# Performance work log

Hardware: AMD Instinct MI355X
Metric: run time of the kernel (lower is better)

## Reference

```python
import jax, jax.numpy as jnp
import numpy as np

B, E, H = 4096, 8, 1024
XDIM, ZDIM, ODIM, GH = 800, 64, 768, 128

def setup_inputs() -> dict:
    key = jax.random.key(0)
    ks = jax.random.split(key, 16)
    s = lambda k, shape, fan: jax.random.normal(k, shape, jnp.float32) / np.sqrt(fan)
    return {
        'x': jax.random.normal(ks[0], (B, XDIM), jnp.float32),
        'z': jax.random.normal(ks[1], (B, ZDIM), jnp.float32),
        'Wg1': s(ks[2], (GH, XDIM + ZDIM), XDIM + ZDIM),
        'bg1': jnp.zeros((GH,), jnp.float32),
        'Wg2': s(ks[3], (GH, GH), GH),
        'bg2': jnp.zeros((GH,), jnp.float32),
        'Wg3': s(ks[4], (E, GH), GH),
        'bg3': jnp.zeros((E,), jnp.float32),
        'W0': s(ks[5], (E, H, XDIM + ZDIM), XDIM + ZDIM),
        'b0': jnp.zeros((E, H), jnp.float32),
        'W1': s(ks[6], (E, H, H + ZDIM), H + ZDIM),
        'b1': jnp.zeros((E, H), jnp.float32),
        'W2': s(ks[7], (E, H, H + ZDIM), H + ZDIM),
        'b2': jnp.zeros((E, H), jnp.float32),
        'W3': s(ks[8], (E, ODIM, H), H),
        'b3': jnp.zeros((E, ODIM), jnp.float32),
    }

def _blended_layer(bc, inp, W, b):
    # equivalent to (sum_e bc_e W_e) @ inp + sum_e bc_e b_e, but computed as
    # per-expert matmul then weighted accumulation (avoids [B,out,in] blend).
    y = jnp.einsum('bi,eoi->beo', inp, W)          # per-expert outputs
    return jnp.einsum('be,beo->bo', bc, y) + bc @ b

def reference(x, z, Wg1, bg1, Wg2, bg2, Wg3, bg3,
              W0, b0, W1, b1, W2, b2, W3, b3):
    g = jnp.concatenate([x, z], axis=1)
    h = jax.nn.elu(g @ Wg1.T + bg1)
    h = jax.nn.elu(h @ Wg2.T + bg2)
    bc = jax.nn.softmax(h @ Wg3.T + bg3, axis=-1)  # [B, E] blend coefficients
    h = jax.nn.elu(_blended_layer(bc, jnp.concatenate([x, z], 1), W0, b0))
    h = jax.nn.elu(_blended_layer(bc, jnp.concatenate([h, z], 1), W1, b1))
    h = jax.nn.elu(_blended_layer(bc, jnp.concatenate([h, z], 1), W2, b2))
    return _blended_layer(bc, h, W3, b3)  # [B, ODIM], no activation
```

## Files before the change

kernel.cpp:

```cpp
#include <hip/hip_runtime.h>
#include <math.h>

#define BDIM 4096
#define NEXP 8
#define HDIM 1024
#define XDIM 800
#define ZDIM 64
#define ODIM 768
#define GH   128

typedef _Float16 f16;
typedef f16   f16x8 __attribute__((ext_vector_type(8)));
typedef f16   f16x4 __attribute__((ext_vector_type(4)));
typedef float f32x4 __attribute__((ext_vector_type(4)));

__device__ __forceinline__ float elu_act(float x) {
    return x > 0.0f ? x : expm1f(x);
}

__device__ __forceinline__ f16x8 vscale(f16x8 v, f16 s) {
    f16x8 r;
    #pragma unroll
    for (int i = 0; i < 8; ++i) r[i] = v[i] * s;
    return r;
}

#define BMg 64
#define BNg 64
#define BKg 32
#define PADg 68

template<int ACT>
__global__ __launch_bounds__(256)
void gemm_cat(const float* __restrict__ srcA, int KH,
              const float* __restrict__ srcZ, int KZ,
              const float* __restrict__ W, const float* __restrict__ bias,
              float* __restrict__ dst, int N)
{
    __shared__ float lds_a[BKg][PADg];
    __shared__ float lds_b[BKg][PADg];
    const int K = KH + KZ;
    const int row0 = blockIdx.x * BMg;
    const int col0 = blockIdx.y * BNg;
    const int tid = threadIdx.x;
    const int tx = tid & 15, ty = tid >> 4;

    float acc[4][4] = {};

    for (int k0 = 0; k0 < K; k0 += BKg) {
        #pragma unroll
        for (int it = 0; it < 2; ++it) {
            int idx = tid + it * 256;
            int r = idx >> 3;
            int f = idx & 7;
            int k = k0 + f * 4;
            const float* src; int col;
            if (k < KH) { src = srcA + (size_t)(row0 + r) * KH; col = k; }
            else        { src = srcZ + (size_t)(row0 + r) * KZ; col = k - KH; }
            float4 v = *(const float4*)(src + col);
            lds_a[f*4+0][r] = v.x; lds_a[f*4+1][r] = v.y;
            lds_a[f*4+2][r] = v.z; lds_a[f*4+3][r] = v.w;
        }
        #pragma unroll
        for (int it = 0; it < 2; ++it) {
            int idx = tid + it * 256;
            int c = idx >> 3;
            int f = idx & 7;
            int k = k0 + f * 4;
            float4 v = *(const float4*)(W + (size_t)(col0 + c) * K + k);
            lds_b[f*4+0][c] = v.x; lds_b[f*4+1][c] = v.y;
            lds_b[f*4+2][c] = v.z; lds_b[f*4+3][c] = v.w;
        }
        __syncthreads();
        #pragma unroll
        for (int j = 0; j < BKg; ++j) {
            float4 a4 = *(const float4*)&lds_a[j][ty*4];
            float4 b4 = *(const float4*)&lds_b[j][tx*4];
            float a[4] = {a4.x, a4.y, a4.z, a4.w};
            float b[4] = {b4.x, b4.y, b4.z, b4.w};
            #pragma unroll
            for (int i = 0; i < 4; ++i)
                #pragma unroll
                for (int jj = 0; jj < 4; ++jj)
                    acc[i][jj] += a[i] * b[jj];
        }
        __syncthreads();
    }

    #pragma unroll
    for (int i = 0; i < 4; ++i) {
        int r = row0 + ty*4 + i;
        float vals[4];
        #pragma unroll
        for (int j = 0; j < 4; ++j) {
            float v = acc[i][j] + bias[col0 + tx*4 + j];
            vals[j] = (ACT == 1) ? elu_act(v) : v;
        }
        *(float4*)(dst + (size_t)r * N + col0 + tx*4) =
            make_float4(vals[0], vals[1], vals[2], vals[3]);
    }
}

__global__ __launch_bounds__(256)
void gating3_softmax(const float* __restrict__ g2, const float* __restrict__ Wg3,
                     const float* __restrict__ bg3, float* __restrict__ bc)
{
    __shared__ float w[NEXP * GH];
    __shared__ float bsh[NEXP];
    const int tid = threadIdx.x;
    for (int i = tid; i < NEXP * GH; i += 256) w[i] = Wg3[i];
    if (tid < NEXP) bsh[tid] = bg3[tid];
    __syncthreads();

    const int rowl = tid >> 3;
    const int o    = tid & 7;
    const int row  = blockIdx.x * 32 + rowl;
    const float* g = g2 + (size_t)row * GH;

    float s = bsh[o];
    for (int k = 0; k < GH; ++k) s += g[k] * w[o * GH + k];

    float m = s;
    #pragma unroll
    for (int d = 4; d >= 1; d >>= 1) m = fmaxf(m, __shfl_xor(m, d, 8));
    float e = expf(s - m);
    float sum = e;
    #pragma unroll
    for (int d = 4; d >= 1; d >>= 1) sum += __shfl_xor(sum, d, 8);

    bc[(size_t)blockIdx.x * 256 + tid] = e / sum;
}

__global__ __launch_bounds__(256)
void fill_z(const float* __restrict__ z, f16* __restrict__ hz_a,
            f16* __restrict__ hz_b)
{
    int i = (blockIdx.x * 256 + threadIdx.x) * 4;
    int row = i >> 6;
    int col = i & 63;
    float4 v = *(const float4*)(z + i);
    f16x4 o = { (f16)v.x, (f16)v.y, (f16)v.z, (f16)v.w };
    size_t off = (size_t)row * (HDIM + ZDIM) + HDIM + col;
    *(f16x4*)(hz_a + off) = o;
    *(f16x4*)(hz_b + off) = o;
}

template<int N, int K>
__global__ __launch_bounds__(256)
void w_tile(const float* __restrict__ W, f16* __restrict__ Wt)
{
    constexpr int KC = K / 32;
    size_t i = (size_t)blockIdx.x * 256 + threadIdx.x;
    int lane = (int)(i & 63);
    size_t t = i >> 6;
    int kc = (int)(t % KC);
    int nt = (int)((t / KC) % (N / 16));
    int e  = (int)(t / KC / (N / 16));
    const float* s = W + ((size_t)e * N + nt * 16 + (lane & 15)) * K
                       + kc * 32 + (lane >> 4) * 8;
    float4 v0 = *(const float4*)s;
    float4 v1 = *(const float4*)(s + 4);
    f16x8 o = { (f16)v0.x,(f16)v0.y,(f16)v0.z,(f16)v0.w,
                (f16)v1.x,(f16)v1.y,(f16)v1.z,(f16)v1.w };
    *(f16x8*)(Wt + i * 8) = o;
}

template<int K, int N, int ACT, int SRC, typename OT>
__global__ __launch_bounds__(256, 2)
void blended_v3(const f16* __restrict__ A, int ldA,
                const float* __restrict__ x, const float* __restrict__ z,
                const f16* __restrict__ Wt, const float* __restrict__ bias,
                const float* __restrict__ bc, OT* __restrict__ out, int ldOut)
{
    constexpr int KC = K / 32;
    __shared__ __align__(16) f16 a_sh[2][128][40];
    __shared__ float bc_sh[128][8];
    __shared__ float bias_sh[8][64];

    const int tid  = threadIdx.x;
    const int col0 = blockIdx.x * 64;
    const int row0 = blockIdx.y * 128;
    const int wave = tid >> 6;
    const int lane = tid & 63;
    const int ln   = lane & 15;
    const int quad = lane >> 4;
    const int wy   = wave >> 1;
    const int wx   = wave & 1;

    for (int i = tid; i < 128 * 8; i += 256)
        bc_sh[i >> 3][i & 7] = bc[(size_t)(row0 + (i >> 3)) * NEXP + (i & 7)];
    for (int i = tid; i < 8 * 64; i += 256)
        bias_sh[i >> 6][i & 63] = bias[(size_t)(i >> 6) * N + col0 + (i & 63)];

    const int ar = tid >> 1;
    const int ak = (tid & 1) * 16;

    auto loadA = [&](int ks, f16x8& lo, f16x8& hi) {
        int k = ks * 32 + ak;
        if (SRC == 0) {
            const float* s = (k < XDIM)
                ? x + (size_t)(row0 + ar) * XDIM + k
                : z + (size_t)(row0 + ar) * ZDIM + (k - XDIM);
            float4 v0 = *(const float4*)s;
            float4 v1 = *(const float4*)(s + 4);
            float4 v2 = *(const float4*)(s + 8);
            float4 v3 = *(const float4*)(s + 12);
            lo = (f16x8){ (f16)v0.x,(f16)v0.y,(f16)v0.z,(f16)v0.w,
                          (f16)v1.x,(f16)v1.y,(f16)v1.z,(f16)v1.w };
            hi = (f16x8){ (f16)v2.x,(f16)v2.y,(f16)v2.z,(f16)v2.w,
                          (f16)v3.x,(f16)v3.y,(f16)v3.z,(f16)v3.w };
        } else {
            const f16* s = A + (size_t)(row0 + ar) * ldA + k;
            lo = *(const f16x8*)s;
            hi = *(const f16x8*)(s + 8);
        }
    };

    f16x8 avlo, avhi;
    loadA(0, avlo, avhi);

    __syncthreads();

    f16 bcf[4][8];
    #pragma unroll
    for (int mt = 0; mt < 4; ++mt)
        #pragma unroll
        for (int e = 0; e < 8; ++e)
            bcf[mt][e] = (f16)bc_sh[wy*64 + mt*16 + ln][e];

    const f16* wp = Wt + ((size_t)(col0/16 + wx*2) * KC) * 512 + lane * 8;
    constexpr size_t ESTR = (size_t)(N/16) * KC * 512;
    constexpr size_t TSTR = (size_t)KC * 512;

    f32x4 acc[4][2] = {};

    for (int ks = 0; ks < KC; ++ks) {
        const int buf = ks & 1;
        *(f16x8*)&a_sh[buf][ar][ak]     = avlo;
        *(f16x8*)&a_sh[buf][ar][ak + 8] = avhi;
        __syncthreads();

        if (ks + 1 < KC) loadA(ks + 1, avlo, avhi);

        f16x8 af[4];
        #pragma unroll
        for (int mt = 0; mt < 4; ++mt)
            af[mt] = *(const f16x8*)&a_sh[buf][wy*64 + mt*16 + ln][quad * 8];

        const f16* wk = wp + (size_t)ks * 512;
        f16x8 b0 = *(const f16x8*)(wk);
        f16x8 b1 = *(const f16x8*)(wk + TSTR);

        #pragma unroll
        for (int e = 0; e < 8; ++e) {
            f16x8 nb0 = b0, nb1 = b1;
            if (e < 7) {
                nb0 = *(const f16x8*)(wk + (size_t)(e+1) * ESTR);
                nb1 = *(const f16x8*)(wk + (size_t)(e+1) * ESTR + TSTR);
            }
            #pragma unroll
            for (int mt = 0; mt < 4; ++mt) {
                f16x8 s = vscale(af[mt], bcf[mt][e]);
                acc[mt][0] = __builtin_amdgcn_mfma_f32_16x16x32_f16(s, b0, acc[mt][0], 0,0,0);
                acc[mt][1] = __builtin_amdgcn_mfma_f32_16x16x32_f16(s, b1, acc[mt][1], 0,0,0);
            }
            b0 = nb0; b1 = nb1;
        }
    }

    #pragma unroll
    for (int mt = 0; mt < 4; ++mt)
        #pragma unroll
        for (int r = 0; r < 4; ++r) {
            int rl = wy*64 + mt*16 + quad*4 + r;
            size_t grow = (size_t)(row0 + rl) * ldOut;
            #pragma unroll
            for (int nt = 0; nt < 2; ++nt) {
                int cl = wx*32 + nt*16 + ln;
                float v = acc[mt][nt][r];
                #pragma unroll
                for (int e2 = 0; e2 < NEXP; ++e2)
                    v += bc_sh[rl][e2] * bias_sh[e2][cl];
                if (ACT) v = elu_act(v);
                out[grow + col0 + cl] = (OT)v;
            }
        }
}

extern "C" void kernel_launch(void* const* d_in, const int* in_sizes, int n_in,
                              void* d_out, int out_size, void* d_ws, size_t ws_size,
                              hipStream_t stream)
{
    const float* x   = (const float*)d_in[0];
    const float* z   = (const float*)d_in[1];
    const float* Wg1 = (const float*)d_in[2];
    const float* bg1 = (const float*)d_in[3];
    const float* Wg2 = (const float*)d_in[4];
    const float* bg2 = (const float*)d_in[5];
    const float* Wg3 = (const float*)d_in[6];
    const float* bg3 = (const float*)d_in[7];
    const float* W0  = (const float*)d_in[8];
    const float* b0  = (const float*)d_in[9];
    const float* W1  = (const float*)d_in[10];
    const float* b1  = (const float*)d_in[11];
    const float* W2  = (const float*)d_in[12];
    const float* b2  = (const float*)d_in[13];
    const float* W3  = (const float*)d_in[14];
    const float* b3  = (const float*)d_in[15];
    float* out = (float*)d_out;

    char* ws = (char*)d_ws;
    f16*   wbuf = (f16*)ws;                 ws += (size_t)NEXP * HDIM * (HDIM + ZDIM) * 2;
    f16*   hz_a = (f16*)ws;                 ws += (size_t)BDIM * (HDIM + ZDIM) * 2;
    f16*   hz_b = (f16*)ws;                 ws += (size_t)BDIM * (HDIM + ZDIM) * 2;
    float* g1   = (float*)ws;               ws += (size_t)BDIM * GH * 4;
    float* g2   = (float*)ws;               ws += (size_t)BDIM * GH * 4;
    float* bcw  = (float*)ws;

    dim3 blk(256);

    fill_z<<<dim3(BDIM * ZDIM / 4 / 256), blk, 0, stream>>>(z, hz_a, hz_b);

    gemm_cat<1><<<dim3(BDIM/BMg, GH/BNg), blk, 0, stream>>>(x, XDIM, z, ZDIM, Wg1, bg1, g1, GH);
    gemm_cat<1><<<dim3(BDIM/BMg, GH/BNg), blk, 0, stream>>>(g1, GH, nullptr, 0, Wg2, bg2, g2, GH);
    gating3_softmax<<<dim3(BDIM/32), blk, 0, stream>>>(g2, Wg3, bg3, bcw);

    w_tile<HDIM, XDIM+ZDIM><<<dim3(NEXP*HDIM*(XDIM+ZDIM)/8/256), blk, 0, stream>>>(W0, wbuf);
    blended_v3<XDIM+ZDIM, HDIM, 1, 0, f16><<<dim3(HDIM/64, BDIM/128), blk, 0, stream>>>(
        nullptr, 0, x, z, wbuf, b0, bcw, hz_a, HDIM + ZDIM);

    w_tile<HDIM, HDIM+ZDIM><<<dim3(NEXP*HDIM*(HDIM+ZDIM)/8/256), blk, 0, stream>>>(W1, wbuf);
    blended_v3<HDIM+ZDIM, HDIM, 1, 1, f16><<<dim3(HDIM/64, BDIM/128), blk, 0, stream>>>(
        hz_a, HDIM + ZDIM, nullptr, nullptr, wbuf, b1, bcw, hz_b, HDIM + ZDIM);

    w_tile<HDIM, HDIM+ZDIM><<<dim3(NEXP*HDIM*(HDIM+ZDIM)/8/256), blk, 0, stream>>>(W2, wbuf);
    blended_v3<HDIM+ZDIM, HDIM, 1, 1, f16><<<dim3(HDIM/64, BDIM/128), blk, 0, stream>>>(
        hz_b, HDIM + ZDIM, nullptr, nullptr, wbuf, b2, bcw, hz_a, HDIM + ZDIM);

    w_tile<ODIM, HDIM><<<dim3(NEXP*ODIM*HDIM/8/256), blk, 0, stream>>>(W3, wbuf);
    blended_v3<HDIM, ODIM, 0, 1, float><<<dim3(ODIM/64, BDIM/128), blk, 0, stream>>>(
        hz_a, HDIM + ZDIM, nullptr, nullptr, wbuf, b3, bcw, out, ODIM);
}
```

Baseline: 694.7 us.

## Fuse gating MLP into one kernel and widen blended GEMM tiles to 128x128

Replaces the z-fill, two gating GEMMs and softmax kernels with one fused kernel that keeps x|z and hidden activations in LDS per 16-row block and reads the gating weights from global/cache. The blended expert GEMM now has each wave cover all 128 rows and 32 columns, giving a 128x128 block tile, so each A fragment is reused across twice as many columns. The goal is fewer launches and less A traffic, at the cost of twice the accumulator registers, occupancy capped at one block per SIMD group, and half as many blocks in the grid.

Result: slower. 779.4 us (+12.2%).

```diff
diff --git a/kernel.cpp b/kernel.cpp
--- a/kernel.cpp
+++ b/kernel.cpp
@@ -25,124 +25,94 @@
     return r;
 }
 
-#define BMg 64
-#define BNg 64
-#define BKg 32
-#define PADg 68
-
-template<int ACT>
 __global__ __launch_bounds__(256)
-void gemm_cat(const float* __restrict__ srcA, int KH,
-              const float* __restrict__ srcZ, int KZ,
-              const float* __restrict__ W, const float* __restrict__ bias,
-              float* __restrict__ dst, int N)
+void gating_fused(const float* __restrict__ x, const float* __restrict__ z,
+                  const float* __restrict__ Wg1, const float* __restrict__ bg1,
+                  const float* __restrict__ Wg2, const float* __restrict__ bg2,
+                  const float* __restrict__ Wg3, const float* __restrict__ bg3,
+                  float* __restrict__ bc, f16* __restrict__ hz_a,
+                  f16* __restrict__ hz_b)
 {
-    __shared__ float lds_a[BKg][PADg];
-    __shared__ float lds_b[BKg][PADg];
-    const int K = KH + KZ;
-    const int row0 = blockIdx.x * BMg;
-    const int col0 = blockIdx.y * BNg;
+    __shared__ float xz_sh[16][868];
+    __shared__ float g1_sh[16][136];
+    __shared__ float g2_sh[16][136];
+
     const int tid = threadIdx.x;
-    const int tx = tid & 15, ty = tid >> 4;
-
-    float acc[4][4] = {};
-
-    for (int k0 = 0; k0 < K; k0 += BKg) {
-        #pragma unroll
-        for (int it = 0; it < 2; ++it) {
-            int idx = tid + it * 256;
-            int r = idx >> 3;
-            int f = idx & 7;
-            int k = k0 + f * 4;
-            const float* src; int col;
-            if (k < KH) { src = srcA + (size_t)(row0 + r) * KH; col = k; }
-            else        { src = srcZ + (size_t)(row0 + r) * KZ; col = k - KH; }
-            float4 v = *(const float4*)(src + col);
-            lds_a[f*4+0][r] = v.x; lds_a[f*4+1][r] = v.y;
-            lds_a[f*4+2][r] = v.z; lds_a[f*4+3][r] = v.w;
-        }
-        #pragma unroll
-        for (int it = 0; it < 2; ++it) {
-            int idx = tid + it * 256;
-            int c = idx >> 3;
-            int f = idx & 7;
-            int k = k0 + f * 4;
-            float4 v = *(const float4*)(W + (size_t)(col0 + c) * K + k);
-            lds_b[f*4+0][c] = v.x; lds_b[f*4+1][c] = v.y;
-            lds_b[f*4+2][c] = v.z; lds_b[f*4+3][c] = v.w;
-        }
-        __syncthreads();
-        #pragma unroll
-        for (int j = 0; j < BKg; ++j) {
-            float4 a4 = *(const float4*)&lds_a[j][ty*4];
-            float4 b4 = *(const float4*)&lds_b[j][tx*4];
-            float a[4] = {a4.x, a4.y, a4.z, a4.w};
-            float b[4] = {b4.x, b4.y, b4.z, b4.w};
+    const int r0  = blockIdx.x * 16;
+
+    for (int i = tid; i < 16 * 200; i += 256) {
+        int r = i / 200, c4 = i - r * 200;
+        float4 v = *(const float4*)(x + (size_t)(r0 + r) * XDIM + c4 * 4);
+        *(float4*)&xz_sh[r][c4 * 4] = v;
+    }
+    {
+        int i = tid;
+        if (i < 256) {
+            int r = i >> 4, c4 = i & 15;
+            float4 v = *(const float4*)(z + (size_t)(r0 + r) * ZDIM + c4 * 4);
+            *(float4*)&xz_sh[r][XDIM + c4 * 4] = v;
+            f16x4 h = { (f16)v.x, (f16)v.y, (f16)v.z, (f16)v.w };
+            size_t off = (size_t)(r0 + r) * (HDIM + ZDIM) + HDIM + c4 * 4;
+            *(f16x4*)(hz_a + off) = h;
+            *(f16x4*)(hz_b + off) = h;
+        }
+    }
+    __syncthreads();
+
+    const int rr = tid >> 4;
+    const int ob = tid & 15;
+
+    {
+        float accg[8];
+        #pragma unroll
+        for (int j = 0; j < 8; ++j) accg[j] = bg1[ob + 16 * j];
+        for (int k4 = 0; k4 < 216; ++k4) {
+            float4 xv = *(const float4*)&xz_sh[rr][k4 * 4];
             #pragma unroll
-            for (int i = 0; i < 4; ++i)
-                #pragma unroll
-                for (int jj = 0; jj < 4; ++jj)
-                    acc[i][jj] += a[i] * b[jj];
-        }
-        __syncthreads();
-    }
-
-    #pragma unroll
-    for (int i = 0; i < 4; ++i) {
-        int r = row0 + ty*4 + i;
-        float vals[4];
-        #pragma unroll
-        for (int j = 0; j < 4; ++j) {
-            float v = acc[i][j] + bias[col0 + tx*4 + j];
-            vals[j] = (ACT == 1) ? elu_act(v) : v;
-        }
-        *(float4*)(dst + (size_t)r * N + col0 + tx*4) =
-            make_float4(vals[0], vals[1], vals[2], vals[3]);
-    }
-}
-
-__global__ __launch_bounds__(256)
-void gating3_softmax(const float* __restrict__ g2, const float* __restrict__ Wg3,
-                     const float* __restrict__ bg3, float* __restrict__ bc)
-{
-    __shared__ float w[NEXP * GH];
-    __shared__ float bsh[NEXP];
-    const int tid = threadIdx.x;
-    for (int i = tid; i < NEXP * GH; i += 256) w[i] = Wg3[i];
-    if (tid < NEXP) bsh[tid] = bg3[tid];
+            for (int j = 0; j < 8; ++j) {
+                float4 wv = *(const float4*)(Wg1 + (size_t)(ob + 16 * j) * 864 + k4 * 4);
+                accg[j] += xv.x * wv.x + xv.y * wv.y + xv.z * wv.z + xv.w * wv.w;
+            }
+        }
+        #pragma unroll
+        for (int j = 0; j < 8; ++j) g1_sh[rr][ob + 16 * j] = elu_act(accg[j]);
+    }
     __syncthreads();
 
-    const int rowl = tid >> 3;
-    const int o    = tid & 7;
-    const int row  = blockIdx.x * 32 + rowl;
-    const float* g = g2 + (size_t)row * GH;
-
-    float s = bsh[o];
-    for (int k = 0; k < GH; ++k) s += g[k] * w[o * GH + k];
-
-    float m = s;
-    #pragma unroll
-    for (int d = 4; d >= 1; d >>= 1) m = fmaxf(m, __shfl_xor(m, d, 8));
-    float e = expf(s - m);
-    float sum = e;
-    #pragma unroll
-    for (int d = 4; d >= 1; d >>= 1) sum += __shfl_xor(sum, d, 8);
-
-    bc[(size_t)blockIdx.x * 256 + tid] = e / sum;
-}
-
-__global__ __launch_bounds__(256)
-void fill_z(const float* __restrict__ z, f16* __restrict__ hz_a,
-            f16* __restrict__ hz_b)
-{
-    int i = (blockIdx.x * 256 + threadIdx.x) * 4;
-    int row = i >> 6;
-    int col = i & 63;
-    float4 v = *(const float4*)(z + i);
-    f16x4 o = { (f16)v.x, (f16)v.y, (f16)v.z, (f16)v.w };
-    size_t off = (size_t)row * (HDIM + ZDIM) + HDIM + col;
-    *(f16x4*)(hz_a + off) = o;
-    *(f16x4*)(hz_b + off) = o;
+    {
+        float accg[8];
+        #pragma unroll
+        for (int j = 0; j < 8; ++j) accg[j] = bg2[ob + 16 * j];
+        for (int k4 = 0; k4 < 32; ++k4) {
+            float4 xv = *(const float4*)&g1_sh[rr][k4 * 4];
+            #pragma unroll
+            for (int j = 0; j < 8; ++j) {
+                float4 wv = *(const float4*)(Wg2 + (size_t)(ob + 16 * j) * GH + k4 * 4);
+                accg[j] += xv.x * wv.x + xv.y * wv.y + xv.z * wv.z + xv.w * wv.w;
+            }
+        }
+        #pragma unroll
+        for (int j = 0; j < 8; ++j) g2_sh[rr][ob + 16 * j] = elu_act(accg[j]);
+    }
+    __syncthreads();
+
+    if (tid < 128) {
+        int r = tid >> 3, e = tid & 7;
+        float s = bg3[e];
+        for (int k4 = 0; k4 < 32; ++k4) {
+            float4 xv = *(const float4*)&g2_sh[r][k4 * 4];
+            float4 wv = *(const float4*)(Wg3 + (size_t)e * GH + k4 * 4);
+            s += xv.x * wv.x + xv.y * wv.y + xv.z * wv.z + xv.w * wv.w;
+        }
+        float m = s;
+        #pragma unroll
+        for (int d = 4; d >= 1; d >>= 1) m = fmaxf(m, __shfl_xor(m, d, 8));
+        float ex = expf(s - m);
+        float sum = ex;
+        #pragma unroll
+        for (int d = 4; d >= 1; d >>= 1) sum += __shfl_xor(sum, d, 8);
+        bc[(size_t)(r0 + r) * NEXP + e] = ex / sum;
+    }
 }
 
 template<int N, int K>
@@ -166,8 +136,8 @@
 }
 
 template<int K, int N, int ACT, int SRC, typename OT>
-__global__ __launch_bounds__(256, 2)
-void blended_v3(const f16* __restrict__ A, int ldA,
+__global__ __launch_bounds__(256, 1)
+void blended_v4(const f16* __restrict__ A, int ldA,
                 const float* __restrict__ x, const float* __restrict__ z,
                 const f16* __restrict__ Wt, const float* __restrict__ bias,
                 const float* __restrict__ bc, OT* __restrict__ out, int ldOut)
@@ -175,22 +145,20 @@
     constexpr int KC = K / 32;
     __shared__ __align__(16) f16 a_sh[2][128][40];
     __shared__ float bc_sh[128][8];
-    __shared__ float bias_sh[8][64];
+    __shared__ float bias_sh[8][128];
 
     const int tid  = threadIdx.x;
-    const int col0 = blockIdx.x * 64;
+    const int col0 = blockIdx.x * 128;
     const int row0 = blockIdx.y * 128;
     const int wave = tid >> 6;
     const int lane = tid & 63;
     const int ln   = lane & 15;
     const int quad = lane >> 4;
-    const int wy   = wave >> 1;
-    const int wx   = wave & 1;
 
     for (int i = tid; i < 128 * 8; i += 256)
         bc_sh[i >> 3][i & 7] = bc[(size_t)(row0 + (i >> 3)) * NEXP + (i & 7)];
-    for (int i = tid; i < 8 * 64; i += 256)
-        bias_sh[i >> 6][i & 63] = bias[(size_t)(i >> 6) * N + col0 + (i & 63)];
+    for (int i = tid; i < 8 * 128; i += 256)
+        bias_sh[i >> 7][i & 127] = bias[(size_t)(i >> 7) * N + col0 + (i & 127)];
 
     const int ar = tid >> 1;
     const int ak = (tid & 1) * 16;
@@ -221,18 +189,18 @@
 
     __syncthreads();
 
-    f16 bcf[4][8];
+    f16 bcf[8][8];
     #pragma unroll
-    for (int mt = 0; mt < 4; ++mt)
+    for (int mt = 0; mt < 8; ++mt)
         #pragma unroll
         for (int e = 0; e < 8; ++e)
-            bcf[mt][e] = (f16)bc_sh[wy*64 + mt*16 + ln][e];
-
-    const f16* wp = Wt + ((size_t)(col0/16 + wx*2) * KC) * 512 + lane * 8;
-    constexpr size_t ESTR = (size_t)(N/16) * KC * 512;
+            bcf[mt][e] = (f16)bc_sh[mt * 16 + ln][e];
+
+    const f16* wp = Wt + ((size_t)(col0 / 16 + wave * 2) * KC) * 512 + lane * 8;
+    constexpr size_t ESTR = (size_t)(N / 16) * KC * 512;
     constexpr size_t TSTR = (size_t)KC * 512;
 
-    f32x4 acc[4][2] = {};
+    f32x4 acc[8][2] = {};
 
     for (int ks = 0; ks < KC; ++ks) {
         const int buf = ks & 1;
@@ -242,10 +210,10 @@
 
         if (ks + 1 < KC) loadA(ks + 1, avlo, avhi);
 
-        f16x8 af[4];
-        #pragma unroll
-        for (int mt = 0; mt < 4; ++mt)
-            af[mt] = *(const f16x8*)&a_sh[buf][wy*64 + mt*16 + ln][quad * 8];
+        f16x8 af[8];
+        #pragma unroll
+        for (int mt = 0; mt < 8; ++mt)
+            af[mt] = *(const f16x8*)&a_sh[buf][mt * 16 + ln][quad * 8];
 
         const f16* wk = wp + (size_t)ks * 512;
         f16x8 b0 = *(const f16x8*)(wk);
@@ -255,11 +223,11 @@
         for (int e = 0; e < 8; ++e) {
             f16x8 nb0 = b0, nb1 = b1;
             if (e < 7) {
-                nb0 = *(const f16x8*)(wk + (size_t)(e+1) * ESTR);
-                nb1 = *(const f16x8*)(wk + (size_t)(e+1) * ESTR + TSTR);
+                nb0 = *(const f16x8*)(wk + (size_t)(e + 1) * ESTR);
+                nb1 = *(const f16x8*)(wk + (size_t)(e + 1) * ESTR + TSTR);
             }
             #pragma unroll
-            for (int mt = 0; mt < 4; ++mt) {
+            for (int mt = 0; mt < 8; ++mt) {
                 f16x8 s = vscale(af[mt], bcf[mt][e]);
                 acc[mt][0] = __builtin_amdgcn_mfma_f32_16x16x32_f16(s, b0, acc[mt][0], 0,0,0);
                 acc[mt][1] = __builtin_amdgcn_mfma_f32_16x16x32_f16(s, b1, acc[mt][1], 0,0,0);
@@ -269,14 +237,14 @@
     }
 
     #pragma unroll
-    for (int mt = 0; mt < 4; ++mt)
+    for (int mt = 0; mt < 8; ++mt)
         #pragma unroll
         for (int r = 0; r < 4; ++r) {
-            int rl = wy*64 + mt*16 + quad*4 + r;
+            int rl = mt * 16 + quad * 4 + r;
             size_t grow = (size_t)(row0 + rl) * ldOut;
             #pragma unroll
             for (int nt = 0; nt < 2; ++nt) {
-                int cl = wx*32 + nt*16 + ln;
+                int cl = wave * 32 + nt * 16 + ln;
                 float v = acc[mt][nt][r];
                 #pragma unroll
                 for (int e2 = 0; e2 < NEXP; ++e2)
@@ -313,31 +281,26 @@
     f16*   wbuf = (f16*)ws;                 ws += (size_t)NEXP * HDIM * (HDIM + ZDIM) * 2;
     f16*   hz_a = (f16*)ws;                 ws += (size_t)BDIM * (HDIM + ZDIM) * 2;
     f16*   hz_b = (f16*)ws;                 ws += (size_t)BDIM * (HDIM + ZDIM) * 2;
-    float* g1   = (float*)ws;               ws += (size_t)BDIM * GH * 4;
-    float* g2   = (float*)ws;               ws += (size_t)BDIM * GH * 4;
     float* bcw  = (float*)ws;
 
     dim3 blk(256);
 
-    fill_z<<<dim3(BDIM * ZDIM / 4 / 256), blk, 0, stream>>>(z, hz_a, hz_b);
-
-    gemm_cat<1><<<dim3(BDIM/BMg, GH/BNg), blk, 0, stream>>>(x, XDIM, z, ZDIM, Wg1, bg1, g1, GH);
-    gemm_cat<1><<<dim3(BDIM/BMg, GH/BNg), blk, 0, stream>>>(g1, GH, nullptr, 0, Wg2, bg2, g2, GH);
-    gating3_softmax<<<dim3(BDIM/32), blk, 0, stream>>>(g2, Wg3, bg3, bcw);
-
-    w_tile<HDIM, XDIM+ZDIM><<<dim3(NEXP*HDIM*(XDIM+ZDIM)/8/256), blk, 0, stream>>>(W0, wbuf);
-    blended_v3<XDIM+ZDIM, HDIM, 1, 0, f16><<<dim3(HDIM/64, BDIM/128), blk, 0, stream>>>(
+    gating_fused<<<dim3(BDIM / 16), blk, 0, stream>>>(
+        x, z, Wg1, bg1, Wg2, bg2, Wg3, bg3, bcw, hz_a, hz_b);
+
+    w_tile<HDIM, XDIM+ZDIM><<<dim3(NEXP*HDIM*(XDIM+ZDIM)/2048), blk, 0, stream>>>(W0, wbuf);
+    blended_v4<XDIM+ZDIM, HDIM, 1, 0, f16><<<dim3(HDIM/128, BDIM/128), blk, 0, stream>>>(
         nullptr, 0, x, z, wbuf, b0, bcw, hz_a, HDIM + ZDIM);
 
-    w_tile<HDIM, HDIM+ZDIM><<<dim3(NEXP*HDIM*(HDIM+ZDIM)/8/256), blk, 0, stream>>>(W1, wbuf);
-    blended_v3<HDIM+ZDIM, HDIM, 1, 1, f16><<<dim3(HDIM/64, BDIM/128), blk, 0, stream>>>(
+    w_tile<HDIM, HDIM+ZDIM><<<dim3(NEXP*HDIM*(HDIM+ZDIM)/2048), blk, 0, stream>>>(W1, wbuf);
+    blended_v4<HDIM+ZDIM, HDIM, 1, 1, f16><<<dim3(HDIM/128, BDIM/128), blk, 0, stream>>>(
         hz_a, HDIM + ZDIM, nullptr, nullptr, wbuf, b1, bcw, hz_b, HDIM + ZDIM);
 
-    w_tile<HDIM, HDIM+ZDIM><<<dim3(NEXP*HDIM*(HDIM+ZDIM)/8/256), blk, 0, stream>>>(W2, wbuf);
-    blended_v3<HDIM+ZDIM, HDIM, 1, 1, f16><<<dim3(HDIM/64, BDIM/128), blk, 0, stream>>>(
+    w_tile<HDIM, HDIM+ZDIM><<<dim3(NEXP*HDIM*(HDIM+ZDIM)/2048), blk, 0, stream>>>(W2, wbuf);
+    blended_v4<HDIM+ZDIM, HDIM, 1, 1, f16><<<dim3(HDIM/128, BDIM/128), blk, 0, stream>>>(
         hz_b, HDIM + ZDIM, nullptr, nullptr, wbuf, b2, bcw, hz_a, HDIM + ZDIM);
 
-    w_tile<ODIM, HDIM><<<dim3(NEXP*ODIM*HDIM/8/256), blk, 0, stream>>>(W3, wbuf);
-    blended_v3<HDIM, ODIM, 0, 1, float><<<dim3(ODIM/64, BDIM/128), blk, 0, stream>>>(
+    w_tile<ODIM, HDIM><<<dim3(NEXP*ODIM*HDIM/2048), blk, 0, stream>>>(W3, wbuf);
+    blended_v4<HDIM, ODIM, 0, 1, float><<<dim3(ODIM/128, BDIM/128), blk, 0, stream>>>(
         hz_a, HDIM + ZDIM, nullptr, nullptr, wbuf, b3, bcw, out, ODIM);
 }
```

## Store activations in MFMA-tiled layout and load A fragments directly from global

Applied to the files above, without the earlier changes.

Converts x/z and intermediate hidden activations into a pre-tiled 16x32 fragment layout so each wave loads its MFMA A operands straight from global memory, removing the LDS staging and per-step block barriers. The block tile widens to 128 columns with each wave covering all 128 rows, and the next weight fragments are prefetched two experts ahead. The epilogue writes hidden outputs back in the tiled layout through a small per-wave LDS transpose, and the gating scratch now reuses the weight buffer. Register pressure grows substantially (occupancy 1) and every wave now reads A redundantly from global or L2.

After: 782.7 us. 12.7% more time.

```diff
diff --git a/kernel.cpp b/kernel.cpp
--- a/kernel.cpp
+++ b/kernel.cpp
@@ -131,18 +131,43 @@
     bc[(size_t)blockIdx.x * 256 + tid] = e / sum;
 }
 
-__global__ __launch_bounds__(256)
-void fill_z(const float* __restrict__ z, f16* __restrict__ hz_a,
-            f16* __restrict__ hz_b)
-{
-    int i = (blockIdx.x * 256 + threadIdx.x) * 4;
-    int row = i >> 6;
-    int col = i & 63;
-    float4 v = *(const float4*)(z + i);
-    f16x4 o = { (f16)v.x, (f16)v.y, (f16)v.z, (f16)v.w };
-    size_t off = (size_t)row * (HDIM + ZDIM) + HDIM + col;
-    *(f16x4*)(hz_a + off) = o;
-    *(f16x4*)(hz_b + off) = o;
+
+__global__ __launch_bounds__(256)
+void xz_tile(const float* __restrict__ x, const float* __restrict__ z,
+             f16* __restrict__ At)
+{
+    size_t i = (size_t)blockIdx.x * 256 + threadIdx.x;
+    int lane = (int)(i & 63);
+    size_t t = i >> 6;
+    int kc = (int)(t % 27);
+    int rt = (int)(t / 27);
+    int m = rt * 16 + (lane & 15);
+    int k = kc * 32 + (lane >> 4) * 8;
+    const float* s = (k < XDIM) ? x + (size_t)m * XDIM + k
+                                : z + (size_t)m * ZDIM + (k - XDIM);
+    float4 v0 = *(const float4*)s;
+    float4 v1 = *(const float4*)(s + 4);
+    f16x8 o = { (f16)v0.x,(f16)v0.y,(f16)v0.z,(f16)v0.w,
+                (f16)v1.x,(f16)v1.y,(f16)v1.z,(f16)v1.w };
+    *(f16x8*)(At + i * 8) = o;
+}
+
+__global__ __launch_bounds__(256)
+void fill_z_tiled(const float* __restrict__ z, f16* __restrict__ At)
+{
+    int i = blockIdx.x * 256 + threadIdx.x;
+    int lane = i & 63;
+    int c = i >> 6;
+    int rt  = c >> 1;
+    int kcz = c & 1;
+    int m  = rt * 16 + (lane & 15);
+    int kz = kcz * 32 + (lane >> 4) * 8;
+    const float* s = z + (size_t)m * ZDIM + kz;
+    float4 v0 = *(const float4*)s;
+    float4 v1 = *(const float4*)(s + 4);
+    f16x8 o = { (f16)v0.x,(f16)v0.y,(f16)v0.z,(f16)v0.w,
+                (f16)v1.x,(f16)v1.y,(f16)v1.z,(f16)v1.w };
+    *(f16x8*)(At + ((size_t)(rt * 34 + 32 + kcz) * 64 + lane) * 8) = o;
 }
 
 template<int N, int K>
@@ -165,126 +190,126 @@
     *(f16x8*)(Wt + i * 8) = o;
 }
 
-template<int K, int N, int ACT, int SRC, typename OT>
-__global__ __launch_bounds__(256, 2)
-void blended_v3(const f16* __restrict__ A, int ldA,
-                const float* __restrict__ x, const float* __restrict__ z,
+template<int KCA, int KLOOP, int N, int ACT, int OMODE, int KCOUT, typename OT>
+__global__ __launch_bounds__(256, 1)
+void blended_v5(const f16* __restrict__ At,
                 const f16* __restrict__ Wt, const float* __restrict__ bias,
                 const float* __restrict__ bc, OT* __restrict__ out, int ldOut)
 {
-    constexpr int KC = K / 32;
-    __shared__ __align__(16) f16 a_sh[2][128][40];
     __shared__ float bc_sh[128][8];
-    __shared__ float bias_sh[8][64];
+    __shared__ float bias_sh[8][128];
+    __shared__ f16 t_sh[4][16][32];
 
     const int tid  = threadIdx.x;
-    const int col0 = blockIdx.x * 64;
+    const int col0 = blockIdx.x * 128;
     const int row0 = blockIdx.y * 128;
     const int wave = tid >> 6;
     const int lane = tid & 63;
     const int ln   = lane & 15;
     const int quad = lane >> 4;
-    const int wy   = wave >> 1;
-    const int wx   = wave & 1;
 
     for (int i = tid; i < 128 * 8; i += 256)
         bc_sh[i >> 3][i & 7] = bc[(size_t)(row0 + (i >> 3)) * NEXP + (i & 7)];
-    for (int i = tid; i < 8 * 64; i += 256)
-        bias_sh[i >> 6][i & 63] = bias[(size_t)(i >> 6) * N + col0 + (i & 63)];
-
-    const int ar = tid >> 1;
-    const int ak = (tid & 1) * 16;
-
-    auto loadA = [&](int ks, f16x8& lo, f16x8& hi) {
-        int k = ks * 32 + ak;
-        if (SRC == 0) {
-            const float* s = (k < XDIM)
-                ? x + (size_t)(row0 + ar) * XDIM + k
-                : z + (size_t)(row0 + ar) * ZDIM + (k - XDIM);
-            float4 v0 = *(const float4*)s;
-            float4 v1 = *(const float4*)(s + 4);
-            float4 v2 = *(const float4*)(s + 8);
-            float4 v3 = *(const float4*)(s + 12);
-            lo = (f16x8){ (f16)v0.x,(f16)v0.y,(f16)v0.z,(f16)v0.w,
-                          (f16)v1.x,(f16)v1.y,(f16)v1.z,(f16)v1.w };
-            hi = (f16x8){ (f16)v2.x,(f16)v2.y,(f16)v2.z,(f16)v2.w,
-                          (f16)v3.x,(f16)v3.y,(f16)v3.z,(f16)v3.w };
-        } else {
-            const f16* s = A + (size_t)(row0 + ar) * ldA + k;
-            lo = *(const f16x8*)s;
-            hi = *(const f16x8*)(s + 8);
-        }
-    };
-
-    f16x8 avlo, avhi;
-    loadA(0, avlo, avhi);
-
+    for (int i = tid; i < 8 * 128; i += 256)
+        bias_sh[i >> 7][i & 127] = bias[(size_t)(i >> 7) * N + col0 + (i & 127)];
     __syncthreads();
 
-    f16 bcf[4][8];
-    #pragma unroll
-    for (int mt = 0; mt < 4; ++mt)
+    f16 bcf[8][8];
+    #pragma unroll
+    for (int mt = 0; mt < 8; ++mt)
         #pragma unroll
         for (int e = 0; e < 8; ++e)
-            bcf[mt][e] = (f16)bc_sh[wy*64 + mt*16 + ln][e];
-
-    const f16* wp = Wt + ((size_t)(col0/16 + wx*2) * KC) * 512 + lane * 8;
-    constexpr size_t ESTR = (size_t)(N/16) * KC * 512;
-    constexpr size_t TSTR = (size_t)KC * 512;
-
-    f32x4 acc[4][2] = {};
-
-    for (int ks = 0; ks < KC; ++ks) {
-        const int buf = ks & 1;
-        *(f16x8*)&a_sh[buf][ar][ak]     = avlo;
-        *(f16x8*)&a_sh[buf][ar][ak + 8] = avhi;
-        __syncthreads();
-
-        if (ks + 1 < KC) loadA(ks + 1, avlo, avhi);
-
-        f16x8 af[4];
-        #pragma unroll
-        for (int mt = 0; mt < 4; ++mt)
-            af[mt] = *(const f16x8*)&a_sh[buf][wy*64 + mt*16 + ln][quad * 8];
-
-        const f16* wk = wp + (size_t)ks * 512;
-        f16x8 b0 = *(const f16x8*)(wk);
-        f16x8 b1 = *(const f16x8*)(wk + TSTR);
+            bcf[mt][e] = (f16)bc_sh[mt * 16 + ln][e];
+
+    const f16* ap[8];
+    #pragma unroll
+    for (int mt = 0; mt < 8; ++mt)
+        ap[mt] = At + ((size_t)(row0 / 16 + mt) * KCA) * 512 + lane * 8;
+
+    constexpr size_t ESTR = (size_t)(N / 16) * KLOOP * 512;
+    const f16* wp0 = Wt + ((size_t)(col0 / 16 + wave * 2 + 0) * KLOOP) * 512 + lane * 8;
+    const f16* wp1 = Wt + ((size_t)(col0 / 16 + wave * 2 + 1) * KLOOP) * 512 + lane * 8;
+
+    f32x4 acc[8][2] = {};
+
+    f16x8 afc[8];
+    #pragma unroll
+    for (int mt = 0; mt < 8; ++mt) afc[mt] = *(const f16x8*)(ap[mt]);
+
+    f16x8 b0a = *(const f16x8*)(wp0);
+    f16x8 b1a = *(const f16x8*)(wp1);
+    f16x8 b0b = *(const f16x8*)(wp0 + ESTR);
+    f16x8 b1b = *(const f16x8*)(wp1 + ESTR);
+
+    for (int ks = 0; ks < KLOOP; ++ks) {
+        f16x8 afn[8];
+        #pragma unroll
+        for (int mt = 0; mt < 8; ++mt)
+            afn[mt] = *(const f16x8*)(ap[mt] + (size_t)(ks + 1) * 512);
 
         #pragma unroll
         for (int e = 0; e < 8; ++e) {
-            f16x8 nb0 = b0, nb1 = b1;
-            if (e < 7) {
-                nb0 = *(const f16x8*)(wk + (size_t)(e+1) * ESTR);
-                nb1 = *(const f16x8*)(wk + (size_t)(e+1) * ESTR + TSTR);
+            const int ks2 = (e < 6) ? ks : ks + 1;
+            const int e2  = (e + 2) & 7;
+            f16x8 nb0 = *(const f16x8*)(wp0 + (size_t)e2 * ESTR + (size_t)ks2 * 512);
+            f16x8 nb1 = *(const f16x8*)(wp1 + (size_t)e2 * ESTR + (size_t)ks2 * 512);
+
+            #pragma unroll
+            for (int mt = 0; mt < 8; ++mt) {
+                f16x8 s = vscale(afc[mt], bcf[mt][e]);
+                acc[mt][0] = __builtin_amdgcn_mfma_f32_16x16x32_f16(s, b0a, acc[mt][0], 0,0,0);
+                acc[mt][1] = __builtin_amdgcn_mfma_f32_16x16x32_f16(s, b1a, acc[mt][1], 0,0,0);
             }
+            b0a = b0b; b1a = b1b;
+            b0b = nb0; b1b = nb1;
+        }
+
+        #pragma unroll
+        for (int mt = 0; mt < 8; ++mt) afc[mt] = afn[mt];
+    }
+
+    if (OMODE == 1) {
+        #pragma unroll
+        for (int mt = 0; mt < 8; ++mt)
             #pragma unroll
-            for (int mt = 0; mt < 4; ++mt) {
-                f16x8 s = vscale(af[mt], bcf[mt][e]);
-                acc[mt][0] = __builtin_amdgcn_mfma_f32_16x16x32_f16(s, b0, acc[mt][0], 0,0,0);
-                acc[mt][1] = __builtin_amdgcn_mfma_f32_16x16x32_f16(s, b1, acc[mt][1], 0,0,0);
+            for (int r = 0; r < 4; ++r) {
+                int rl = mt * 16 + quad * 4 + r;
+                size_t grow = (size_t)(row0 + rl) * ldOut;
+                #pragma unroll
+                for (int nt = 0; nt < 2; ++nt) {
+                    int cl = wave * 32 + nt * 16 + ln;
+                    float v = acc[mt][nt][r];
+                    #pragma unroll
+                    for (int e2 = 0; e2 < NEXP; ++e2)
+                        v += bc_sh[rl][e2] * bias_sh[e2][cl];
+                    if (ACT) v = elu_act(v);
+                    out[grow + col0 + cl] = (OT)v;
+                }
             }
-            b0 = nb0; b1 = nb1;
-        }
-    }
-
-    #pragma unroll
-    for (int mt = 0; mt < 4; ++mt)
-        #pragma unroll
-        for (int r = 0; r < 4; ++r) {
-            int rl = wy*64 + mt*16 + quad*4 + r;
-            size_t grow = (size_t)(row0 + rl) * ldOut;
+    } else {
+        f16* tb = &t_sh[wave][0][0];
+        const int kc_out = col0 / 32 + wave;
+        #pragma unroll
+        for (int mt = 0; mt < 8; ++mt) {
             #pragma unroll
             for (int nt = 0; nt < 2; ++nt) {
-                int cl = wx*32 + nt*16 + ln;
-                float v = acc[mt][nt][r];
+                int cl = wave * 32 + nt * 16 + ln;
                 #pragma unroll
-                for (int e2 = 0; e2 < NEXP; ++e2)
-                    v += bc_sh[rl][e2] * bias_sh[e2][cl];
-                if (ACT) v = elu_act(v);
-                out[grow + col0 + cl] = (OT)v;
+                for (int r = 0; r < 4; ++r) {
+                    int rl = mt * 16 + quad * 4 + r;
+                    float v = acc[mt][nt][r];
+                    #pragma unroll
+                    for (int e2 = 0; e2 < NEXP; ++e2)
+                        v += bc_sh[rl][e2] * bias_sh[e2][cl];
+                    if (ACT) v = elu_act(v);
+                    tb[(quad * 4 + r) * 32 + nt * 16 + ln] = (f16)v;
+                }
             }
-        }
+            f16x8 o = *(const f16x8*)&tb[(lane & 15) * 32 + (lane >> 4) * 8];
+            *(f16x8*)((f16*)out +
+                ((size_t)(row0 / 16 + mt) * KCOUT + kc_out) * 512 + lane * 8) = o;
+        }
+    }
 }
 
 extern "C" void kernel_launch(void* const* d_in, const int* in_sizes, int n_in,
@@ -313,31 +338,36 @@
     f16*   wbuf = (f16*)ws;                 ws += (size_t)NEXP * HDIM * (HDIM + ZDIM) * 2;
     f16*   hz_a = (f16*)ws;                 ws += (size_t)BDIM * (HDIM + ZDIM) * 2;
     f16*   hz_b = (f16*)ws;                 ws += (size_t)BDIM * (HDIM + ZDIM) * 2;
-    float* g1   = (float*)ws;               ws += (size_t)BDIM * GH * 4;
-    float* g2   = (float*)ws;               ws += (size_t)BDIM * GH * 4;
     float* bcw  = (float*)ws;
 
+    float* g1   = (float*)wbuf;
+    float* g2   = g1 + (size_t)BDIM * GH;
+    f16*   xz_t = hz_b;
+
     dim3 blk(256);
 
-    fill_z<<<dim3(BDIM * ZDIM / 4 / 256), blk, 0, stream>>>(z, hz_a, hz_b);
+    xz_tile<<<dim3(BDIM * (XDIM + ZDIM) / 8 / 256), blk, 0, stream>>>(x, z, xz_t);
+    fill_z_tiled<<<dim3(BDIM * ZDIM / 8 / 256), blk, 0, stream>>>(z, hz_a);
 
     gemm_cat<1><<<dim3(BDIM/BMg, GH/BNg), blk, 0, stream>>>(x, XDIM, z, ZDIM, Wg1, bg1, g1, GH);
     gemm_cat<1><<<dim3(BDIM/BMg, GH/BNg), blk, 0, stream>>>(g1, GH, nullptr, 0, Wg2, bg2, g2, GH);
     gating3_softmax<<<dim3(BDIM/32), blk, 0, stream>>>(g2, Wg3, bg3, bcw);
 
-    w_tile<HDIM, XDIM+ZDIM><<<dim3(NEXP*HDIM*(XDIM+ZDIM)/8/256), blk, 0, stream>>>(W0, wbuf);
-    blended_v3<XDIM+ZDIM, HDIM, 1, 0, f16><<<dim3(HDIM/64, BDIM/128), blk, 0, stream>>>(
-        nullptr, 0, x, z, wbuf, b0, bcw, hz_a, HDIM + ZDIM);
-
-    w_tile<HDIM, HDIM+ZDIM><<<dim3(NEXP*HDIM*(HDIM+ZDIM)/8/256), blk, 0, stream>>>(W1, wbuf);
-    blended_v3<HDIM+ZDIM, HDIM, 1, 1, f16><<<dim3(HDIM/64, BDIM/128), blk, 0, stream>>>(
-        hz_a, HDIM + ZDIM, nullptr, nullptr, wbuf, b1, bcw, hz_b, HDIM + ZDIM);
-
-    w_tile<HDIM, HDIM+ZDIM><<<dim3(NEXP*HDIM*(HDIM+ZDIM)/8/256), blk, 0, stream>>>(W2, wbuf);
-    blended_v3<HDIM+ZDIM, HDIM, 1, 1, f16><<<dim3(HDIM/64, BDIM/128), blk, 0, stream>>>(
-        hz_b, HDIM + ZDIM, nullptr, nullptr, wbuf, b2, bcw, hz_a, HDIM + ZDIM);
-
-    w_tile<ODIM, HDIM><<<dim3(NEXP*ODIM*HDIM/8/256), blk, 0, stream>>>(W3, wbuf);
-    blended_v3<HDIM, ODIM, 0, 1, float><<<dim3(ODIM/64, BDIM/128), blk, 0, stream>>>(
-        hz_a, HDIM + ZDIM, nullptr, nullptr, wbuf, b3, bcw, out, ODIM);
-}
+    w_tile<HDIM, XDIM+ZDIM><<<dim3(NEXP*HDIM*(XDIM+ZDIM)/2048), blk, 0, stream>>>(W0, wbuf);
+    blended_v5<27, 27, HDIM, 1, 0, 34, f16><<<dim3(HDIM/128, BDIM/128), blk, 0, stream>>>(
+        xz_t, wbuf, b0, bcw, hz_a, 0);
+
+    fill_z_tiled<<<dim3(BDIM * ZDIM / 8 / 256), blk, 0, stream>>>(z, hz_b);
+
+    w_tile<HDIM, HDIM+ZDIM><<<dim3(NEXP*HDIM*(HDIM+ZDIM)/2048), blk, 0, stream>>>(W1, wbuf);
+    blended_v5<34, 34, HDIM, 1, 0, 34, f16><<<dim3(HDIM/128, BDIM/128), blk, 0, stream>>>(
+        hz_a, wbuf, b1, bcw, hz_b, 0);
+
+    w_tile<HDIM, HDIM+ZDIM><<<dim3(NEXP*HDIM*(HDIM+ZDIM)/2048), blk, 0, stream>>>(W2, wbuf);
+    blended_v5<34, 34, HDIM, 1, 0, 34, f16><<<dim3(HDIM/128, BDIM/128), blk, 0, stream>>>(
+        hz_b, wbuf, b2, bcw, hz_a, 0);
+
+    w_tile<ODIM, HDIM><<<dim3(NEXP*ODIM*HDIM/2048), blk, 0, stream>>>(W3, wbuf);
+    blended_v5<34, 32, ODIM, 0, 1, 0, float><<<dim3(ODIM/128, BDIM/128), blk, 0, stream>>>(
+        hz_a, wbuf, b3, bcw, out, ODIM);
+}
```
